# Kernel optimization log

Hardware: AMD Instinct MI355X
Metric: run time of the kernel (lower is better)

The kernel has to match this reference:

```python
import jax, jax.numpy as jnp
import numpy as np

B, T, HID = 4, 16, 4096
H, D = 32, 128
S_PAST = 4096


def setup_inputs() -> dict:
    key = jax.random.key(0)
    ks = jax.random.split(key, 7)
    w_scale = 0.02  # keep logits/activations numerically tame
    return {
        "hidden": jax.random.normal(ks[0], (B, T, HID), dtype=jnp.float32),
        "cache_k": jax.random.normal(ks[1], (B, H, S_PAST, D), dtype=jnp.float32),
        "cache_v": jax.random.normal(ks[2], (B, H, S_PAST, D), dtype=jnp.float32),
        "wq": jax.random.normal(ks[3], (HID, HID), dtype=jnp.float32) * w_scale,
        "wk": jax.random.normal(ks[4], (HID, HID), dtype=jnp.float32) * w_scale,
        "wv": jax.random.normal(ks[5], (HID, HID), dtype=jnp.float32) * w_scale,
        "wo": jax.random.normal(ks[6], (HID, HID), dtype=jnp.float32) * w_scale,
    }


def reference(hidden, cache_k, cache_v, wq, wk, wv, wo):
    b, t, _ = hidden.shape
    # QKV projections (torch Linear: x @ W.T), reshape to [B,H,T,D]
    q = (hidden @ wq.T).reshape(b, t, H, D).transpose(0, 2, 1, 3)
    k_new = (hidden @ wk.T).reshape(b, t, H, D).transpose(0, 2, 1, 3)
    v_new = (hidden @ wv.T).reshape(b, t, H, D).transpose(0, 2, 1, 3)
    # DynamicCache append-by-concat
    k_full = jnp.concatenate([cache_k, k_new], axis=2)  # [B,H,S+T,D]
    v_full = jnp.concatenate([cache_v, v_new], axis=2)
    # SDPA, non-causal (torch default), scale = 1/sqrt(D)
    scale = 1.0 / jnp.sqrt(jnp.asarray(D, dtype=q.dtype))
    scores = jnp.einsum("bhtd,bhsd->bhts", q, k_full) * scale
    attn = jax.nn.softmax(scores, axis=-1)
    ctx = jnp.einsum("bhts,bhsd->bhtd", attn, v_full)  # [B,H,T,D]
    out = ctx.transpose(0, 2, 1, 3).reshape(b, t, H * D) @ wo.T
    return out, k_full, v_full
```

## Files before the change

kernel.cpp:

```cpp
#include <hip/hip_runtime.h>
#include <hip/hip_bf16.h>
#include <math.h>

#define HIDN  4096
#define NH    32
#define HD    128
#define NB    4
#define NT    16
#define SPAST 4096
#define STOT  4112
#define NCHUNK 8

#define WS_Q    0
#define WS_CTX  262144
#define WS_PART 524288
#define PART_STRIDE 2080

typedef float f32x4 __attribute__((ext_vector_type(4)));
typedef short bf16x8 __attribute__((ext_vector_type(8)));

__device__ __forceinline__ bf16x8 load_bf16x8(const float* p) {
    const float4* p4 = (const float4*)p;
    float4 a = p4[0], b = p4[1];
    union { __hip_bfloat162 h[4]; bf16x8 v; } r;
    r.h[0] = __float22bfloat162_rn(make_float2(a.x, a.y));
    r.h[1] = __float22bfloat162_rn(make_float2(a.z, a.w));
    r.h[2] = __float22bfloat162_rn(make_float2(b.x, b.y));
    r.h[3] = __float22bfloat162_rn(make_float2(b.z, b.w));
    return r.v;
}

__global__ __launch_bounds__(256) void gemm64_kernel(
    const float* __restrict__ A,
    const float* __restrict__ w0, const float* __restrict__ w1, const float* __restrict__ w2,
    float* __restrict__ c0, float* __restrict__ c1, float* __restrict__ c2)
{
    const int mi   = threadIdx.x >> 6;
    const int lane = threadIdx.x & 63;
    const int l16  = lane & 15;
    const int quad = lane >> 4;
    const int y = blockIdx.y;
    const float* W = (y == 0) ? w0 : (y == 1) ? w1 : w2;
    float*       C = (y == 0) ? c0 : (y == 1) ? c1 : c2;

    const int n = blockIdx.x * 16 + l16;
    const float* wrow = W + (size_t)n * HIDN + quad * 8;
    const float* arow = A + (size_t)(mi * 16 + l16) * HIDN + quad * 8;

    f32x4 acc = {};
#pragma unroll 4
    for (int k0 = 0; k0 < HIDN; k0 += 32) {
        bf16x8 bfrag = load_bf16x8(wrow + k0);
        bf16x8 afrag = load_bf16x8(arow + k0);
        acc = __builtin_amdgcn_mfma_f32_16x16x32_bf16(afrag, bfrag, acc, 0, 0, 0);
    }
#pragma unroll
    for (int r = 0; r < 4; ++r) {
        int m = mi * 16 + quad * 4 + r;
        if (y == 0) {
            C[(size_t)m * HIDN + n] = acc[r];
        } else {
            int b = m >> 4, t = m & 15, h = n >> 7, d = n & 127;
            C[((size_t)(b * NH + h) * STOT + SPAST + t) * HD + d] = acc[r];
        }
    }
}

__global__ __launch_bounds__(256) void attn_partial_kernel(
    const float* __restrict__ qp,
    const float* __restrict__ ck,
    const float* __restrict__ cv,
    float* __restrict__ kf,
    float* __restrict__ vf,
    float* __restrict__ part)
{
    __shared__ float qs[16][128];
    __shared__ float sc[16][257];
    __shared__ float red[16][16];
    __shared__ float m_run[16], l_run[16], alpha_s[16];

    const int tid = threadIdx.x;
    const int bh  = blockIdx.x;
    const int c   = blockIdx.y;
    const int b = bh >> 5, h = bh & 31;
    const int s_beg = c * 512;
    const int s_end = (c == NCHUNK - 1) ? STOT : (s_beg + 512);

    const float scale = 0.08838834764831845f;
    for (int i = tid; i < 16 * 128; i += 256) {
        int t = i >> 7, d = i & 127;
        qs[t][d] = qp[(size_t)(b * 16 + t) * HIDN + h * 128 + d] * scale;
    }
    if (tid < 16) { m_run[tid] = -INFINITY; l_run[tid] = 0.f; }
    __syncthreads();

    const int tg = tid >> 4;
    const int ig = tid & 15;
    float o_loc[8];
#pragma unroll
    for (int i = 0; i < 8; ++i) o_loc[i] = 0.f;

    for (int s0 = s_beg; s0 < s_end; s0 += 256) {
        const int tile_n = min(256, s_end - s0);
        const bool is_new = (s0 >= SPAST);
        if (tid < tile_n) {
            const int s = s0 + tid;
            const float* krow = is_new ? (kf + ((size_t)bh * STOT  + s) * HD)
                                       : (ck + ((size_t)bh * SPAST + s) * HD);
            float* kdst = kf + ((size_t)bh * STOT + s) * HD;
            float scr[16];
#pragma unroll
            for (int t = 0; t < 16; ++t) scr[t] = 0.f;
            for (int dc = 0; dc < 128; dc += 32) {
                float4 kb[8];
#pragma unroll
                for (int u = 0; u < 8; ++u) kb[u] = ((const float4*)(krow + dc))[u];
                if (!is_new) {
#pragma unroll
                    for (int u = 0; u < 8; ++u) ((float4*)(kdst + dc))[u] = kb[u];
                }
#pragma unroll
                for (int t = 0; t < 16; ++t) {
                    float s4 = 0.f;
#pragma unroll
                    for (int u = 0; u < 8; ++u) {
                        float4 qv = ((const float4*)&qs[t][dc])[u];
                        s4 += qv.x * kb[u].x + qv.y * kb[u].y + qv.z * kb[u].z + qv.w * kb[u].w;
                    }
                    scr[t] += s4;
                }
            }
#pragma unroll
            for (int t = 0; t < 16; ++t) sc[t][tid] = scr[t];
        }
        __syncthreads();
        {
            float pm = -INFINITY;
            for (int j = ig; j < tile_n; j += 16) pm = fmaxf(pm, sc[tg][j]);
            red[tg][ig] = pm;
        }
        __syncthreads();
        if (tid < 16) {
            float tmax = -INFINITY;
#pragma unroll
            for (int i = 0; i < 16; ++i) tmax = fmaxf(tmax, red[tid][i]);
            float mo = m_run[tid];
            float mn = fmaxf(mo, tmax);
            alpha_s[tid] = __expf(mo - mn);
            m_run[tid] = mn;
        }
        __syncthreads();
        {
            float ps = 0.f;
            const float mn = m_run[tg];
            for (int j = ig; j < tile_n; j += 16) {
                float p = __expf(sc[tg][j] - mn);
                sc[tg][j] = p;
                ps += p;
            }
            red[tg][ig] = ps;
        }
        __syncthreads();
        if (tid < 16) {
            float ts = 0.f;
#pragma unroll
            for (int i = 0; i < 16; ++i) ts += red[tid][i];
            l_run[tid] = l_run[tid] * alpha_s[tid] + ts;
        }
        __syncthreads();
        {
            const float al = alpha_s[tg];
#pragma unroll
            for (int i = 0; i < 8; ++i) o_loc[i] *= al;
            const float* vsrc = is_new ? (vf + ((size_t)bh * STOT  + s0) * HD)
                                       : (cv + ((size_t)bh * SPAST + s0) * HD);
            float* vdst = vf + ((size_t)bh * STOT + s0) * HD;
            for (int j = 0; j < tile_n; ++j) {
                float p = sc[tg][j];
                const float4* vr = (const float4*)(vsrc + (size_t)j * HD + ig * 8);
                float4 v0 = vr[0], v1 = vr[1];
                if (!is_new && ((j & 15) == tg)) {
                    float4* vw = (float4*)(vdst + (size_t)j * HD + ig * 8);
                    vw[0] = v0; vw[1] = v1;
                }
                o_loc[0] += p * v0.x; o_loc[1] += p * v0.y;
                o_loc[2] += p * v0.z; o_loc[3] += p * v0.w;
                o_loc[4] += p * v1.x; o_loc[5] += p * v1.y;
                o_loc[6] += p * v1.z; o_loc[7] += p * v1.w;
            }
        }
        __syncthreads();
    }
    float* pp = part + ((size_t)bh * NCHUNK + c) * PART_STRIDE;
#pragma unroll
    for (int i = 0; i < 8; ++i) pp[tg * 128 + ig * 8 + i] = o_loc[i];
    if (tid < 16) { pp[2048 + tid] = m_run[tid]; pp[2064 + tid] = l_run[tid]; }
}

__global__ __launch_bounds__(256) void combine_kernel(
    const float* __restrict__ part, float* __restrict__ ctx)
{
    const int bh = blockIdx.x;
    const int tid = threadIdx.x;
    const int t = tid >> 4, i = tid & 15;
    const int b = bh >> 5, h = bh & 31;
    const float* pb = part + (size_t)bh * NCHUNK * PART_STRIDE;

    float M = -INFINITY;
#pragma unroll
    for (int cI = 0; cI < NCHUNK; ++cI) M = fmaxf(M, pb[cI * PART_STRIDE + 2048 + t]);
    float L = 0.f;
    float w[NCHUNK];
#pragma unroll
    for (int cI = 0; cI < NCHUNK; ++cI) {
        float e = __expf(pb[cI * PART_STRIDE + 2048 + t] - M);
        w[cI] = e;
        L += e * pb[cI * PART_STRIDE + 2064 + t];
    }
    const float invL = 1.f / L;
    float o[8];
#pragma unroll
    for (int k = 0; k < 8; ++k) o[k] = 0.f;
#pragma unroll
    for (int cI = 0; cI < NCHUNK; ++cI) {
        const float* po = pb + cI * PART_STRIDE + t * 128 + i * 8;
        const float wc = w[cI];
#pragma unroll
        for (int k = 0; k < 8; ++k) o[k] += wc * po[k];
    }
    float* dst = ctx + (size_t)(b * 16 + t) * HIDN + h * 128 + i * 8;
#pragma unroll
    for (int k = 0; k < 8; ++k) dst[k] = o[k] * invL;
}

extern "C" void kernel_launch(void* const* d_in, const int* in_sizes, int n_in,
                              void* d_out, int out_size, void* d_ws, size_t ws_size,
                              hipStream_t stream) {
    const float* hidden  = (const float*)d_in[0];
    const float* cache_k = (const float*)d_in[1];
    const float* cache_v = (const float*)d_in[2];
    const float* wq = (const float*)d_in[3];
    const float* wk = (const float*)d_in[4];
    const float* wv = (const float*)d_in[5];
    const float* wo = (const float*)d_in[6];

    float* out   = (float*)d_out;
    float* kfull = out + 262144;
    float* vfull = kfull + 67371008LL;

    float* ws   = (float*)d_ws;
    float* qp   = ws + WS_Q;
    float* ctx  = ws + WS_CTX;
    float* part = ws + WS_PART;

    gemm64_kernel<<<dim3(256, 3), 256, 0, stream>>>(hidden, wq, wk, wv, qp, kfull, vfull);
    attn_partial_kernel<<<dim3(128, NCHUNK), 256, 0, stream>>>(
        qp, cache_k, cache_v, kfull, vfull, part);
    combine_kernel<<<dim3(128), 256, 0, stream>>>(part, ctx);
    gemm64_kernel<<<dim3(256, 1), 256, 0, stream>>>(ctx, wo, wo, wo, out, nullptr, nullptr);
}
```

Baseline: 1.419 ms.

## Split attention into more chunks and spread K rows across four lanes

Raises the number of sequence chunks from 8 to 12 (344 rows each) so more blocks run concurrently, and adds an occupancy hint to the launch bounds. The K dot product is now split across 4 lanes per key row, each reading interleaved float4 slices, with shuffle reductions combining them. This gives coalesced K loads and fewer registers per thread. The V loop reads probabilities as float4 and picks the cache or new-K source per row, so tiles that straddle the past/new boundary are handled correctly. Costs are extra shuffles and more partials for the combine step, and the combine kernel must use the new NCHUNK.

```diff
diff --git a/kernel.cpp b/kernel.cpp
--- a/kernel.cpp
+++ b/kernel.cpp
@@ -9,7 +9,8 @@
 #define NT    16
 #define SPAST 4096
 #define STOT  4112
-#define NCHUNK 8
+#define NCHUNK 12
+#define CHUNK 344
 
 #define WS_Q    0
 #define WS_CTX  262144
@@ -66,7 +67,7 @@
     }
 }
 
-__global__ __launch_bounds__(256) void attn_partial_kernel(
+__global__ __launch_bounds__(256, 6) void attn_partial_kernel(
     const float* __restrict__ qp,
     const float* __restrict__ ck,
     const float* __restrict__ cv,
@@ -75,7 +76,7 @@
     float* __restrict__ part)
 {
     __shared__ float qs[16][128];
-    __shared__ float sc[16][257];
+    __shared__ float sc[16][260];
     __shared__ float red[16][16];
     __shared__ float m_run[16], l_run[16], alpha_s[16];
 
@@ -83,8 +84,8 @@
     const int bh  = blockIdx.x;
     const int c   = blockIdx.y;
     const int b = bh >> 5, h = bh & 31;
-    const int s_beg = c * 512;
-    const int s_end = (c == NCHUNK - 1) ? STOT : (s_beg + 512);
+    const int s_beg = c * CHUNK;
+    const int s_end = min(s_beg + CHUNK, STOT);
 
     const float scale = 0.08838834764831845f;
     for (int i = tid; i < 16 * 128; i += 256) {
@@ -96,42 +97,43 @@
 
     const int tg = tid >> 4;
     const int ig = tid & 15;
+    const int q4 = tid & 3;
     float o_loc[8];
 #pragma unroll
     for (int i = 0; i < 8; ++i) o_loc[i] = 0.f;
 
     for (int s0 = s_beg; s0 < s_end; s0 += 256) {
         const int tile_n = min(256, s_end - s0);
-        const bool is_new = (s0 >= SPAST);
-        if (tid < tile_n) {
-            const int s = s0 + tid;
-            const float* krow = is_new ? (kf + ((size_t)bh * STOT  + s) * HD)
-                                       : (ck + ((size_t)bh * SPAST + s) * HD);
-            float* kdst = kf + ((size_t)bh * STOT + s) * HD;
-            float scr[16];
-#pragma unroll
-            for (int t = 0; t < 16; ++t) scr[t] = 0.f;
-            for (int dc = 0; dc < 128; dc += 32) {
+#pragma unroll
+        for (int s_sub = 0; s_sub < 4; ++s_sub) {
+            const int j = s_sub * 64 + (tid >> 2);
+            if (j < tile_n) {
+                const int s = s0 + j;
+                const float* krow = (s < SPAST) ? (ck + ((size_t)bh * SPAST + s) * HD)
+                                                : (kf + ((size_t)bh * STOT  + s) * HD);
                 float4 kb[8];
 #pragma unroll
-                for (int u = 0; u < 8; ++u) kb[u] = ((const float4*)(krow + dc))[u];
-                if (!is_new) {
-#pragma unroll
-                    for (int u = 0; u < 8; ++u) ((float4*)(kdst + dc))[u] = kb[u];
+                for (int u = 0; u < 8; ++u)
+                    kb[u] = *(const float4*)(krow + u * 16 + q4 * 4);
+                if (s < SPAST) {
+                    float* kdst = kf + ((size_t)bh * STOT + s) * HD;
+#pragma unroll
+                    for (int u = 0; u < 8; ++u)
+                        *(float4*)(kdst + u * 16 + q4 * 4) = kb[u];
                 }
 #pragma unroll
                 for (int t = 0; t < 16; ++t) {
                     float s4 = 0.f;
 #pragma unroll
                     for (int u = 0; u < 8; ++u) {
-                        float4 qv = ((const float4*)&qs[t][dc])[u];
+                        float4 qv = *(const float4*)(&qs[t][u * 16 + q4 * 4]);
                         s4 += qv.x * kb[u].x + qv.y * kb[u].y + qv.z * kb[u].z + qv.w * kb[u].w;
                     }
-                    scr[t] += s4;
+                    s4 += __shfl_xor(s4, 1, 64);
+                    s4 += __shfl_xor(s4, 2, 64);
+                    if (q4 == 0) sc[t][j] = s4;
                 }
             }
-#pragma unroll
-            for (int t = 0; t < 16; ++t) sc[t][tid] = scr[t];
         }
         __syncthreads();
         {
@@ -172,21 +174,26 @@
             const float al = alpha_s[tg];
 #pragma unroll
             for (int i = 0; i < 8; ++i) o_loc[i] *= al;
-            const float* vsrc = is_new ? (vf + ((size_t)bh * STOT  + s0) * HD)
-                                       : (cv + ((size_t)bh * SPAST + s0) * HD);
-            float* vdst = vf + ((size_t)bh * STOT + s0) * HD;
-            for (int j = 0; j < tile_n; ++j) {
-                float p = sc[tg][j];
-                const float4* vr = (const float4*)(vsrc + (size_t)j * HD + ig * 8);
-                float4 v0 = vr[0], v1 = vr[1];
-                if (!is_new && ((j & 15) == tg)) {
-                    float4* vw = (float4*)(vdst + (size_t)j * HD + ig * 8);
-                    vw[0] = v0; vw[1] = v1;
+            for (int j0 = 0; j0 < tile_n; j0 += 4) {
+                float4 p4 = *(const float4*)&sc[tg][j0];
+#pragma unroll
+                for (int jj = 0; jj < 4; ++jj) {
+                    const int j = j0 + jj;
+                    const int s = s0 + j;
+                    const float p = (jj == 0) ? p4.x : (jj == 1) ? p4.y : (jj == 2) ? p4.z : p4.w;
+                    const float* vrow = (s < SPAST) ? (cv + ((size_t)bh * SPAST + s) * HD)
+                                                    : (vf + ((size_t)bh * STOT  + s) * HD);
+                    const float4* vr = (const float4*)(vrow + ig * 8);
+                    float4 v0 = vr[0], v1 = vr[1];
+                    if (s < SPAST && ((j & 15) == tg)) {
+                        float4* vw = (float4*)(vf + ((size_t)bh * STOT + s) * HD + ig * 8);
+                        vw[0] = v0; vw[1] = v1;
+                    }
+                    o_loc[0] += p * v0.x; o_loc[1] += p * v0.y;
+                    o_loc[2] += p * v0.z; o_loc[3] += p * v0.w;
+                    o_loc[4] += p * v1.x; o_loc[5] += p * v1.y;
+                    o_loc[6] += p * v1.z; o_loc[7] += p * v1.w;
                 }
-                o_loc[0] += p * v0.x; o_loc[1] += p * v0.y;
-                o_loc[2] += p * v0.z; o_loc[3] += p * v0.w;
-                o_loc[4] += p * v1.x; o_loc[5] += p * v1.y;
-                o_loc[6] += p * v1.z; o_loc[7] += p * v1.w;
             }
         }
         __syncthreads();
```

Result: faster. 1.358 ms (-4.3%).
